# Performance work log

Measured on AMD Instinct MI355X. Metric: run time of the kernel, lower is better.

The kernel has to match this reference:

```python
import jax, jax.numpy as jnp
import numpy as np

EPS = 1e-8


def setup_inputs() -> dict:
    key = jax.random.key(0)
    k1, k2, k3 = jax.random.split(key, 3)
    n_nodes, n_pos, d, n_seg = 50000, 2048, 128, 32
    pred = jax.random.normal(k1, (n_nodes, d), dtype=jnp.float32)
    target = jax.random.normal(k2, (n_pos, d), dtype=jnp.float32)
    target_identifiers = jax.random.randint(k3, (n_pos,), 0, n_seg, dtype=jnp.int64)
    return {
        "pred": pred,
        "target": target,
        "target_identifiers": target_identifiers,
        "num_segments": n_seg,
    }


def reference(pred, target, target_identifiers, num_segments):
    # Pairwise L2 distance: sqrt(||t||^2 - 2 t.p + ||p||^2 + eps)
    # avoids materializing the [n_pos, n_nodes, d] broadcast tensor.
    t2 = jnp.sum(target * target, axis=-1, keepdims=True)          # [n_pos, 1]
    p2 = jnp.sum(pred * pred, axis=-1)                             # [n_nodes]
    cross = jnp.einsum('pd,nd->pn', target, pred)                  # [n_pos, n_nodes]
    sq = jnp.maximum(t2 - 2.0 * cross + p2[None, :], 0.0)
    dist_mat = jnp.sqrt(sq + EPS)                                  # [n_pos, n_nodes]

    # stage1: scatter_mean over target_identifiers (dim=0)
    seg_sum = jax.ops.segment_sum(dist_mat, target_identifiers,
                                  num_segments=num_segments)       # [n_seg, n_nodes]
    counts = jax.ops.segment_sum(jnp.ones((dist_mat.shape[0],), dist_mat.dtype),
                                 target_identifiers, num_segments=num_segments)
    seg_mean = seg_sum / jnp.maximum(counts, 1.0)[:, None]

    # stage2: mean over segments
    return seg_mean.mean(axis=0)                                   # [n_nodes]
```

## Files before the change

kernel.cpp:

```cpp
#include <hip/hip_runtime.h>

#define DIMK 128
#define SLICE_TILES 8
#define NODES_PER_BLOCK 128

typedef __bf16 bf16x8 __attribute__((ext_vector_type(8)));
typedef float  f32x4  __attribute__((ext_vector_type(4)));

__device__ inline unsigned short f32_to_bf16_rne(float f) {
    unsigned u = __float_as_uint(f);
    u += 0x7FFFu + ((u >> 16) & 1u);
    return (unsigned short)(u >> 16);
}


__global__ void pack_rows(const float* __restrict__ src,
                          unsigned short* __restrict__ dst,
                          float* __restrict__ norm2,
                          int n_valid, int n_rows_pad, float scale) {
    int wave = threadIdx.x >> 6, lane = threadIdx.x & 63;
    int row = blockIdx.x * 4 + wave;
    if (row >= n_rows_pad) return;
    int srow = min(row, n_valid - 1);
    int e = lane * 2;
    float2 v = *(const float2*)(src + (size_t)srow * DIMK + e);
    unsigned pk = (unsigned)f32_to_bf16_rne(scale * v.x) |
                  ((unsigned)f32_to_bf16_rne(scale * v.y) << 16);
    int tile = row >> 4, col = row & 15;
    int kk = e >> 5, kb = (e >> 3) & 3, j = e & 7;
    size_t off = (size_t)tile * 2048 + kk * 512 + (kb * 16 + col) * 8 + j;
    *(unsigned*)(dst + off) = pk;
    float s = v.x * v.x + v.y * v.y;
#pragma unroll
    for (int o = 1; o < 64; o <<= 1) s += __shfl_xor(s, o, 64);
    if (lane == 0) norm2[row] = s;
}

__global__ void seg_weights(const int* __restrict__ ids,
                            const int* __restrict__ nseg_p,
                            float* __restrict__ wsa, int n_pos) {
    __shared__ int   cnt[256];
    __shared__ float w[256];
    int nseg = nseg_p[0];
    if (nseg > 256) nseg = 256;
    int t = threadIdx.x;
    if (t < nseg) cnt[t] = 0;
    __syncthreads();
    for (int p = t; p < n_pos; p += blockDim.x) atomicAdd(&cnt[ids[p]], 1);
    __syncthreads();
    if (t < nseg) w[t] = 1.0f / ((float)nseg * (float)max(cnt[t], 1));
    __syncthreads();
    for (int p = t; p < n_pos; p += blockDim.x) wsa[p] = w[ids[p]];
}

__global__ __launch_bounds__(256, 4)
void l2dist_main(const unsigned short* __restrict__ pb,
                 const float* __restrict__ p2,
                 const unsigned short* __restrict__ tb,
                 const float* __restrict__ t2g,
                 const float* __restrict__ wg,
                 float* __restrict__ out,
                 int n_nodes) {
    __shared__ __align__(16) unsigned short lbuf[SLICE_TILES][2048];
    __shared__ __align__(16) float t2_lds[SLICE_TILES * 16];
    __shared__ __align__(16) float w_lds[SLICE_TILES * 16];

    const int tid  = threadIdx.x;
    const int lane = tid & 63;
    const int wave = tid >> 6;
    const int col  = lane & 15;
    const int kb   = lane >> 4;
    const int n0   = blockIdx.y * NODES_PER_BLOCK + wave * 32;

    const int pbase = blockIdx.x * SLICE_TILES;
    const unsigned short* sgp = tb + (size_t)pbase * 2048 + wave * 512 + lane * 8;
    unsigned short* ldst = &lbuf[0][0] + wave * 512;
#pragma unroll
    for (int t = 0; t < SLICE_TILES; ++t) {
        __builtin_amdgcn_global_load_lds(
            (const __attribute__((address_space(1))) unsigned int*)(const void*)
                (sgp + (size_t)t * 2048),
            (__attribute__((address_space(3))) unsigned int*)(void*)
                (ldst + t * 2048),
            16, 0, 0);
    }

    if (tid < SLICE_TILES * 16) {
        t2_lds[tid] = t2g[pbase * 16 + tid];
        w_lds[tid]  = wg[pbase * 16 + tid];
    }

    bf16x8 bfrag[2][4];
    float p2g[2];
    const unsigned short* bp = pb + ((size_t)(n0 >> 4)) * 2048 + (size_t)lane * 8;
#pragma unroll
    for (int g = 0; g < 2; ++g) {
#pragma unroll
        for (int kk = 0; kk < 4; ++kk)
            bfrag[g][kk] = *(const bf16x8*)(bp + g * 2048 + kk * 512);
        p2g[g] = p2[n0 + g * 16 + col];
    }

    __syncthreads();

    float acc0 = 0.f, acc1 = 0.f;
#pragma unroll
    for (int t = 0; t < SLICE_TILES; ++t) {
        const int te = (t + 2 * wave) & (SLICE_TILES - 1);

        const unsigned short* rb = &lbuf[te][lane * 8];
        bf16x8 a0 = *(const bf16x8*)(rb);
        bf16x8 a1 = *(const bf16x8*)(rb + 512);
        bf16x8 a2 = *(const bf16x8*)(rb + 1024);
        bf16x8 a3 = *(const bf16x8*)(rb + 1536);

        f32x4 t2v = *(const f32x4*)&t2_lds[te * 16 + kb * 4];
        f32x4 wv  = *(const f32x4*)&w_lds[te * 16 + kb * 4];

        f32x4 d0a = t2v + p2g[0];
        f32x4 d1a = t2v + p2g[1];
        f32x4 d0b = {0.f, 0.f, 0.f, 0.f};
        f32x4 d1b = {0.f, 0.f, 0.f, 0.f};
        d0a = __builtin_amdgcn_mfma_f32_16x16x32_bf16(a0, bfrag[0][0], d0a, 0, 0, 0);
        d1a = __builtin_amdgcn_mfma_f32_16x16x32_bf16(a0, bfrag[1][0], d1a, 0, 0, 0);
        d0b = __builtin_amdgcn_mfma_f32_16x16x32_bf16(a2, bfrag[0][2], d0b, 0, 0, 0);
        d1b = __builtin_amdgcn_mfma_f32_16x16x32_bf16(a2, bfrag[1][2], d1b, 0, 0, 0);
        d0a = __builtin_amdgcn_mfma_f32_16x16x32_bf16(a1, bfrag[0][1], d0a, 0, 0, 0);
        d1a = __builtin_amdgcn_mfma_f32_16x16x32_bf16(a1, bfrag[1][1], d1a, 0, 0, 0);
        d0b = __builtin_amdgcn_mfma_f32_16x16x32_bf16(a3, bfrag[0][3], d0b, 0, 0, 0);
        d1b = __builtin_amdgcn_mfma_f32_16x16x32_bf16(a3, bfrag[1][3], d1b, 0, 0, 0);

        f32x4 s0 = d0a + d0b;
        f32x4 s1 = d1a + d1b;
#pragma unroll
        for (int j = 0; j < 4; ++j) {
            acc0 = fmaf(wv[j], __builtin_amdgcn_sqrtf(fmaxf(s0[j], 0.f)), acc0);
            acc1 = fmaf(wv[j], __builtin_amdgcn_sqrtf(fmaxf(s1[j], 0.f)), acc1);
        }
    }

    acc0 += __shfl_xor(acc0, 16, 64);
    acc0 += __shfl_xor(acc0, 32, 64);
    acc1 += __shfl_xor(acc1, 16, 64);
    acc1 += __shfl_xor(acc1, 32, 64);
    if (lane < 16) {
        int na = n0 + col;
        if (na      < n_nodes) atomicAdd(out + na,      acc0);
        if (na + 16 < n_nodes) atomicAdd(out + na + 16, acc1);
    }
}

extern "C" void kernel_launch(void* const* d_in, const int* in_sizes, int n_in,
                              void* d_out, int out_size, void* d_ws, size_t ws_size,
                              hipStream_t stream) {
    const float* pred  = (const float*)d_in[0];
    const float* tgt   = (const float*)d_in[1];
    const int*   ids   = (const int*)d_in[2];
    const int*   nsegp = (const int*)d_in[3];
    float* out = (float*)d_out;

    int n_nodes = in_sizes[0] / DIMK;
    int n_pos   = in_sizes[2];

    int gy = (n_nodes + NODES_PER_BLOCK - 1) / NODES_PER_BLOCK;
    int n_rows_pad = gy * NODES_PER_BLOCK;

    char* ws = (char*)d_ws;
    size_t off_pb = 0;
    size_t off_tb = off_pb + (size_t)n_rows_pad * DIMK * 2;
    size_t off_p2 = off_tb + (size_t)n_pos * DIMK * 2;
    size_t off_t2 = off_p2 + (size_t)n_rows_pad * 4;
    size_t off_w  = off_t2 + (size_t)n_pos * 4;
    unsigned short* pb  = (unsigned short*)(ws + off_pb);
    unsigned short* tb  = (unsigned short*)(ws + off_tb);
    float*          p2  = (float*)(ws + off_p2);
    float*          t2  = (float*)(ws + off_t2);
    float*          wsa = (float*)(ws + off_w);

    pack_rows<<<(n_rows_pad + 3) / 4, 256, 0, stream>>>(pred, pb, p2, n_nodes, n_rows_pad, 1.0f);
    pack_rows<<<(n_pos + 3) / 4, 256, 0, stream>>>(tgt, tb, t2, n_pos, n_pos, -2.0f);
    seg_weights<<<1, 1024, 0, stream>>>(ids, nsegp, wsa, n_pos);
    hipMemsetAsync(out, 0, (size_t)out_size * sizeof(float), stream);

    int gx = (n_pos >> 4) / SLICE_TILES;
    dim3 grid(gx, gy);
    l2dist_main<<<grid, 256, 0, stream>>>(pb, p2, tb, t2, wsa, out, n_nodes);
}
```

Baseline: 56.07 us.

## Merge pred/target packing into one launch and halve slice tiles per block

The two pack_rows launches are fused into a single pack_all kernel that handles pred rows and then target rows, removing one kernel launch. The main kernel now uses 4 target tiles per block instead of 8, which doubles the grid in x and halves LDS per block, and launch bounds are raised to 6 blocks per CU. The intent is to cut launch overhead and raise occupancy. In exchange, each pred fragment load is reused over fewer target tiles and twice as many atomic adds go to the output.

```diff
diff --git a/kernel.cpp b/kernel.cpp
--- a/kernel.cpp
+++ b/kernel.cpp
@@ -1,7 +1,7 @@
 #include <hip/hip_runtime.h>
 
 #define DIMK 128
-#define SLICE_TILES 8
+#define SLICE_TILES 4
 #define NODES_PER_BLOCK 128
 
 typedef __bf16 bf16x8 __attribute__((ext_vector_type(8)));
@@ -14,26 +14,38 @@
 }
 
 
-__global__ void pack_rows(const float* __restrict__ src,
-                          unsigned short* __restrict__ dst,
-                          float* __restrict__ norm2,
-                          int n_valid, int n_rows_pad, float scale) {
+__global__ void pack_all(const float* __restrict__ pred,
+                         const float* __restrict__ tgt,
+                         unsigned short* __restrict__ pb,
+                         unsigned short* __restrict__ tb,
+                         float* __restrict__ p2,
+                         float* __restrict__ t2,
+                         int n_nodes, int n_rows_pad, int n_pos) {
     int wave = threadIdx.x >> 6, lane = threadIdx.x & 63;
     int row = blockIdx.x * 4 + wave;
-    if (row >= n_rows_pad) return;
-    int srow = min(row, n_valid - 1);
+
+    const float* src; unsigned short* dst; float* nrm; float scale; int r;
+    if (row < n_rows_pad) {
+        src = pred + (size_t)min(row, n_nodes - 1) * DIMK;
+        dst = pb; nrm = p2; scale = 1.0f; r = row;
+    } else {
+        int trow = row - n_rows_pad;
+        if (trow >= n_pos) return;
+        src = tgt + (size_t)trow * DIMK;
+        dst = tb; nrm = t2; scale = -2.0f; r = trow;
+    }
     int e = lane * 2;
-    float2 v = *(const float2*)(src + (size_t)srow * DIMK + e);
+    float2 v = *(const float2*)(src + e);
     unsigned pk = (unsigned)f32_to_bf16_rne(scale * v.x) |
                   ((unsigned)f32_to_bf16_rne(scale * v.y) << 16);
-    int tile = row >> 4, col = row & 15;
+    int tile = r >> 4, col = r & 15;
     int kk = e >> 5, kb = (e >> 3) & 3, j = e & 7;
     size_t off = (size_t)tile * 2048 + kk * 512 + (kb * 16 + col) * 8 + j;
     *(unsigned*)(dst + off) = pk;
     float s = v.x * v.x + v.y * v.y;
 #pragma unroll
     for (int o = 1; o < 64; o <<= 1) s += __shfl_xor(s, o, 64);
-    if (lane == 0) norm2[row] = s;
+    if (lane == 0) nrm[r] = s;
 }
 
 __global__ void seg_weights(const int* __restrict__ ids,
@@ -53,7 +65,7 @@
     for (int p = t; p < n_pos; p += blockDim.x) wsa[p] = w[ids[p]];
 }
 
-__global__ __launch_bounds__(256, 4)
+__global__ __launch_bounds__(256, 6)
 void l2dist_main(const unsigned short* __restrict__ pb,
                  const float* __restrict__ p2,
                  const unsigned short* __restrict__ tb,
@@ -106,7 +118,7 @@
     float acc0 = 0.f, acc1 = 0.f;
 #pragma unroll
     for (int t = 0; t < SLICE_TILES; ++t) {
-        const int te = (t + 2 * wave) & (SLICE_TILES - 1);
+        const int te = (t + wave) & (SLICE_TILES - 1);
 
         const unsigned short* rb = &lbuf[te][lane * 8];
         bf16x8 a0 = *(const bf16x8*)(rb);
@@ -177,8 +189,9 @@
     float*          t2  = (float*)(ws + off_t2);
     float*          wsa = (float*)(ws + off_w);
 
-    pack_rows<<<(n_rows_pad + 3) / 4, 256, 0, stream>>>(pred, pb, p2, n_nodes, n_rows_pad, 1.0f);
-    pack_rows<<<(n_pos + 3) / 4, 256, 0, stream>>>(tgt, tb, t2, n_pos, n_pos, -2.0f);
+    int prows = n_rows_pad + n_pos;
+    pack_all<<<(prows + 3) / 4, 256, 0, stream>>>(pred, tgt, pb, tb, p2, t2,
+                                                  n_nodes, n_rows_pad, n_pos);
     seg_weights<<<1, 1024, 0, stream>>>(ids, nsegp, wsa, n_pos);
     hipMemsetAsync(out, 0, (size_t)out_size * sizeof(float), stream);
 
```

Result: no change. 56.15 us (+0.1%).
